# Optimization experiments

Measured on AMD Instinct MI355X. Metric: run time of the kernel, lower is better.

## Reference

```python
import jax, jax.numpy as jnp
import numpy as np

SIZE_DICT = 512
DIM_DICT = 256
TEMPERATURE = 0.5
EPS = 1e-10


def setup_inputs() -> dict:
    key = jax.random.key(0)
    k1, k2, k3 = jax.random.split(key, 3)
    bs, dim_z, W, H = 32, DIM_DICT, 32, 32
    z_from_encoder = jax.random.normal(k1, (bs, dim_z, W, H), dtype=jnp.float32)
    kappa_q = jnp.ones((1,), dtype=jnp.float32)
    codebook = jax.random.normal(k2, (SIZE_DICT, DIM_DICT), dtype=jnp.float32)
    gumbel_u = jax.random.uniform(k3, (bs * W * H, SIZE_DICT), dtype=jnp.float32)
    return {"z_from_encoder": z_from_encoder, "kappa_q": kappa_q,
            "codebook": codebook, "gumbel_u": gumbel_u, "flg_train": 1}


def reference(z_from_encoder, kappa_q, codebook, gumbel_u, flg_train):
    bs, dim_z, W, H = z_from_encoder.shape
    # [bs, dim_z, W, H] -> [bs*W*H, dim_z]
    z_flat = jnp.transpose(z_from_encoder, (0, 2, 3, 1)).reshape(-1, dim_z)
    kq = jnp.clip(kappa_q, 1e-5, 1e5)  # scalar-ish [1]
    # L2-normalize codebook rows
    cb = codebook / jnp.linalg.norm(codebook, axis=1, keepdims=True)
    # logit = -distance = kappa * <z, c>   [N, K]
    logit = kq * (z_flat @ cb.T)
    logit = logit - jnp.max(logit, axis=-1, keepdims=True)
    logit = jnp.clip(logit, -50.0, 50.0)
    probabilities = jax.nn.softmax(logit, axis=-1)
    log_probabilities = jax.nn.log_softmax(logit, axis=-1)
    # training path: gumbel-softmax relaxation
    g = -jnp.log(-jnp.log(gumbel_u + EPS) + EPS)
    encodings = jax.nn.softmax((logit + g) / TEMPERATURE, axis=-1)
    z_quantized = (encodings @ cb).reshape(bs, W, H, dim_z)
    avg_probs = jnp.mean(jax.lax.stop_gradient(probabilities), axis=0)
    z_to_decoder = jnp.transpose(z_quantized, (0, 3, 1, 2))
    kld_discrete = jnp.sum(probabilities * log_probabilities) / bs
    kld_continuous = jnp.mean(
        jnp.sum(z_from_encoder * (z_from_encoder - z_to_decoder) * kq[0],
                axis=(1, 2, 3)))
    loss = kld_discrete + kld_continuous
    avg_probs = jnp.clip(avg_probs, 1e-10, None)
    perplexity = jnp.exp(-jnp.sum(avg_probs * jnp.log(avg_probs + 1e-10)))
    return z_to_decoder, loss, perplexity
```

## Files before the change

### kernel.cpp

```cpp
#include <hip/hip_runtime.h>
#include <stdint.h>


typedef float v4f __attribute__((ext_vector_type(4)));
typedef short v8s __attribute__((ext_vector_type(8)));
typedef short v4s __attribute__((ext_vector_type(4)));

#define ZA_STR 264
#define L2_STR 520
#define EC_STR 40

__device__ __forceinline__ uint16_t f2bf(float x) {
  uint32_t u = __float_as_uint(x);
  u = u + 0x7fffu + ((u >> 16) & 1u);
  return (uint16_t)(u >> 16);
}
__device__ __forceinline__ float bf2f(uint16_t h) {
  return __uint_as_float(((uint32_t)h) << 16);
}


__global__ __launch_bounds__(64) void vq_prep0(const float* __restrict__ cb,
                                               char* __restrict__ ws) {
  const int blk = blockIdx.x, t = threadIdx.x;
  float* shadow = (float*)(ws + 524288);
  float* scal   = (float*)(ws + 557056);
  float* rnorm  = (float*)(ws + 557072);
  if (blk < 512) {
    float s = 0.f;
#pragma unroll
    for (int i = 0; i < 4; i++) { const float v = cb[blk * 256 + t + 64 * i]; s += v * v; }
#pragma unroll
    for (int mm = 1; mm < 64; mm <<= 1) s += __shfl_xor(s, mm, 64);
    if (t == 0) rnorm[blk] = 1.0f / sqrtf(s);
  } else if (blk < 528) {
    const int j = blk - 512;
#pragma unroll
    for (int i = 0; i < 8; i++) shadow[j * 512 + t + 64 * i] = 0.f;
  } else {
    if (t < 3) scal[t] = 0.f;
  }
}

__global__ __launch_bounds__(256) void vq_prep1(const float* __restrict__ cb,
                                                char* __restrict__ ws) {
  const int b = blockIdx.x, t = threadIdx.x;
  uint16_t* cbn2 = (uint16_t*)ws;
  uint16_t* cbt2 = (uint16_t*)(ws + 262144);
  const float* rnorm = (const float*)(ws + 557072);
  union { v8s v; uint16_t u[8]; } pk;
  if (b < 64) {
    const int g = b * 256 + t;
    const int code = g >> 5, dch = g & 31;
    const float rn = rnorm[code];
    const float4 f0 = *(const float4*)(cb + code * 256 + dch * 8);
    const float4 f1 = *(const float4*)(cb + code * 256 + dch * 8 + 4);
    pk.u[0] = f2bf(f0.x * rn); pk.u[1] = f2bf(f0.y * rn);
    pk.u[2] = f2bf(f0.z * rn); pk.u[3] = f2bf(f0.w * rn);
    pk.u[4] = f2bf(f1.x * rn); pk.u[5] = f2bf(f1.y * rn);
    pk.u[6] = f2bf(f1.z * rn); pk.u[7] = f2bf(f1.w * rn);
    const int w = code >> 7, ct = (code >> 4) & 7, mcol = code & 15;
    const int ks = dch >> 2, q3 = dch & 3;
    *(v8s*)(cbn2 + ((ks * 8 + ct) * 4 + w) * 512 + (q3 * 16 + mcol) * 8) = pk.v;
  } else {
    const int g = (b - 64) * 256 + t;
    const int cgroup = g >> 8, d = g & 255;
#pragma unroll
    for (int j = 0; j < 8; j++) {
      const int c = cgroup * 8 + j;
      pk.u[j] = f2bf(cb[c * 256 + d] * rnorm[c]);
    }
    const int cc = cgroup >> 2, qq = cgroup & 3;
    const int wd = d >> 6, nt = (d >> 4) & 3, md = d & 15;
    *(v8s*)(cbt2 + ((cc * 4 + nt) * 4 + wd) * 512 + (qq * 16 + md) * 8) = pk.v;
  }
}

__global__ __launch_bounds__(256, 4) void vq_main(const float* __restrict__ z,
                                                  const float* __restrict__ kappa,
                                                  const float* __restrict__ gum,
                                                  char* __restrict__ ws,
                                                  float* __restrict__ out) {
  __shared__ char s_A[33280];
  __shared__ char s_B[5120];
  __shared__ float s_M[32], s_rS[32], s_kd[32], s_rSe[32], s_red[8];

  const int t = threadIdx.x;
  const int w = t >> 6, lane = t & 63, q = lane >> 4, m = lane & 15;
  const int bi = blockIdx.x, b = bi >> 5, wh0 = (bi & 31) << 5;
  const int R0 = bi << 5;

  const uint16_t* cbn2 = (const uint16_t*)ws;
  const uint16_t* cbt2 = (const uint16_t*)(ws + 262144);
  float* shadow = (float*)(ws + 524288);
  float* scal   = (float*)(ws + 557056);

  uint16_t* za  = (uint16_t*)s_A;
  uint16_t* l2s = (uint16_t*)s_A;
  float* s_pm = (float*)s_B;
  float* s_pS = (float*)s_B + 128;
  float* s_pT = (float*)s_B + 256;
  short* s_ec = (short*)s_B;

  const float kq = fminf(fmaxf(kappa[0], 1e-5f), 1e5f);

  const int row = t >> 3, c4 = (t & 7) << 2;
  const float* gbase = gum + (size_t)(R0 + row) * 512 + c4;

  {
    float zs = 0.f;
    const int whb = (t & 7) << 2, dT = t >> 3;
    const float* zb = z + ((size_t)b << 18) + wh0 + whb;
#pragma unroll
    for (int s = 0; s < 8; s++) {
      const int d = dT + (s << 5);
      const float4 v = *(const float4*)(zb + (d << 10));
      zs += v.x * v.x + v.y * v.y + v.z * v.z + v.w * v.w;
      za[(whb + 0) * ZA_STR + d] = f2bf(v.x);
      za[(whb + 1) * ZA_STR + d] = f2bf(v.y);
      za[(whb + 2) * ZA_STR + d] = f2bf(v.z);
      za[(whb + 3) * ZA_STR + d] = f2bf(v.w);
    }
#pragma unroll
    for (int mm = 1; mm < 64; mm <<= 1) zs += __shfl_xor(zs, mm, 64);
    if (lane == 0) s_red[w] = zs;
  }

  float4 gq[4];
#pragma unroll
  for (int i = 0; i < 4; i++) gq[i] = *(const float4*)(gbase + (i << 5));

  __syncthreads();
  if (t == 0) atomicAdd(&scal[1], s_red[0] + s_red[1] + s_red[2] + s_red[3]);

  v4f acc0[8], acc1[8];
#pragma unroll
  for (int i = 0; i < 8; i++) { acc0[i] = (v4f)0.f; acc1[i] = (v4f)0.f; }
  {
    const uint16_t* bp  = cbn2 + (w << 9) + (lane << 3);
    const uint16_t* a0p = za + m * ZA_STR;
    const uint16_t* a1p = za + (m + 16) * ZA_STR;
#pragma unroll
    for (int ks = 0; ks < 8; ks++) {
      const v8s a0 = *(const v8s*)(a0p + (ks << 5) + (q << 3));
      const v8s a1 = *(const v8s*)(a1p + (ks << 5) + (q << 3));
#pragma unroll
      for (int ct = 0; ct < 8; ct++) {
        const v8s bf = *(const v8s*)(bp + (((ks << 3) + ct) << 11));
        acc0[ct] = __builtin_amdgcn_mfma_f32_16x16x32_bf16(a0, bf, acc0[ct], 0, 0, 0);
        acc1[ct] = __builtin_amdgcn_mfma_f32_16x16x32_bf16(a1, bf, acc1[ct], 0, 0, 0);
      }
    }
  }
#pragma unroll
  for (int i = 0; i < 8; i++) { acc0[i] *= kq; acc1[i] *= kq; }

  {
    auto stats_half = [&](v4f (&acc)[8], int half) {
#pragma unroll
      for (int reg = 0; reg < 4; reg++) {
        float mx = -1e30f;
#pragma unroll
        for (int ct = 0; ct < 8; ct++) mx = fmaxf(mx, acc[ct][reg]);
#pragma unroll
        for (int mm = 1; mm < 16; mm <<= 1) mx = fmaxf(mx, __shfl_xor(mx, mm, 64));
        float S = 0.f, T = 0.f;
#pragma unroll
        for (int ct = 0; ct < 8; ct++) {
          const float d = acc[ct][reg] - mx;
          const float e = __expf(d);
          S += e; T += d * e;
        }
#pragma unroll
        for (int mm = 1; mm < 16; mm <<= 1) { S += __shfl_xor(S, mm, 64); T += __shfl_xor(T, mm, 64); }
        if (m == 0) {
          const int r = half * 16 + q * 4 + reg;
          s_pm[(w << 5) + r] = mx; s_pS[(w << 5) + r] = S; s_pT[(w << 5) + r] = T;
        }
      }
    };
    stats_half(acc0, 0);
    stats_half(acc1, 1);
  }
  __syncthreads();
  if (t < 32) {
    float M = s_pm[t];
    M = fmaxf(M, s_pm[32 + t]); M = fmaxf(M, s_pm[64 + t]); M = fmaxf(M, s_pm[96 + t]);
    float S = 0.f, T = 0.f;
#pragma unroll
    for (int ww = 0; ww < 4; ww++) {
      const float dm = s_pm[ww * 32 + t] - M;
      const float al = __expf(dm);
      S += s_pS[ww * 32 + t] * al;
      T += (s_pT[ww * 32 + t] + dm * s_pS[ww * 32 + t]) * al;
    }
    const float rS = 1.0f / S;
    s_M[t] = M; s_rS[t] = rS; s_kd[t] = T * rS - __logf(S);
  }
  __syncthreads();

  {
    const int c0 = w << 7;
    float colacc[8];
#pragma unroll
    for (int i = 0; i < 8; i++) colacc[i] = 0.f;
    auto pass2_half = [&](v4f (&acc)[8], int half) {
#pragma unroll
      for (int reg = 0; reg < 4; reg++) {
        const int r = half * 16 + q * 4 + reg;
        const float Mr = s_M[r], rSr = s_rS[r];
        uint16_t* lrow = l2s + r * L2_STR + c0 + m;
#pragma unroll
        for (int ct = 0; ct < 8; ct++) {
          const float d = fmaxf(acc[ct][reg] - Mr, -50.0f);
          const float e = __expf(d);
          colacc[ct] += e * rSr;
          lrow[ct << 4] = f2bf(d);
        }
      }
    };
    pass2_half(acc0, 0);
    pass2_half(acc1, 1);
#pragma unroll
    for (int i = 0; i < 8; i++) {
      colacc[i] += __shfl_xor(colacc[i], 16, 64);
      colacc[i] += __shfl_xor(colacc[i], 32, 64);
    }
    if (q == 0) {
      float* sh = shadow + ((bi & 15) << 9) + c0 + m;
#pragma unroll
      for (int i = 0; i < 8; i++) atomicAdd(&sh[i << 4], colacc[i]);
    }
    if (w == 0) {
      float kd = s_kd[lane & 31];
#pragma unroll
      for (int mm = 1; mm < 64; mm <<= 1) kd += __shfl_xor(kd, mm, 64);
      if (lane == 0) atomicAdd(&scal[0], 0.5f * kd);
    }
  }
  __syncthreads();

  const float mxr = s_M[row];
  float se = 0.f, ce = 0.f;
  v4f acc2a[4], acc2b[4];
#pragma unroll
  for (int i = 0; i < 4; i++) { acc2a[i] = (v4f)0.f; acc2b[i] = (v4f)0.f; }

  auto compute_chunk = [&](int cc) {
    const int buf = cc & 1;
    const float4 u = gq[cc & 3];
    const float uu[4] = {u.x, u.y, u.z, u.w};
    union { v4s v; uint16_t h[4]; } lv, eb;
    lv.v = *(const v4s*)(l2s + row * L2_STR + (cc << 5) + c4);
#pragma unroll
    for (int i = 0; i < 4; i++) {
      const float l2 = bf2f(lv.h[i]);
      const float L = -__logf(uu[i] + 1e-10f) + 1e-10f;
      const float er = __expf(2.0f * (l2 - __logf(L)));
      se += er; ce += er * (l2 + mxr);
      eb.h[i] = f2bf(er);
    }
    *(v4s*)(s_ec + buf * 1280 + row * EC_STR + c4) = eb.v;
    if (cc + 4 < 16) gq[cc & 3] = *(const float4*)(gbase + ((cc + 4) << 5));
  };
  auto mfma_chunk = [&](int cc) {
    const int buf = cc & 1;
    const v8s a0 = *(const v8s*)(s_ec + buf * 1280 + m * EC_STR + (q << 3));
    const v8s a1 = *(const v8s*)(s_ec + buf * 1280 + (m + 16) * EC_STR + (q << 3));
    const uint16_t* bp2 = cbt2 + (cc << 13) + (w << 9) + (lane << 3);
#pragma unroll
    for (int nt = 0; nt < 4; nt++) {
      const v8s bf = *(const v8s*)(bp2 + (nt << 11));
      acc2a[nt] = __builtin_amdgcn_mfma_f32_16x16x32_bf16(a0, bf, acc2a[nt], 0, 0, 0);
      acc2b[nt] = __builtin_amdgcn_mfma_f32_16x16x32_bf16(a1, bf, acc2b[nt], 0, 0, 0);
    }
  };

  compute_chunk(0);
  __syncthreads();
#pragma unroll
  for (int cc = 0; cc < 16; cc++) {
    mfma_chunk(cc);
    if (cc < 15) compute_chunk(cc + 1);
    __syncthreads();
  }

#pragma unroll
  for (int mm = 1; mm < 8; mm <<= 1) { se += __shfl_xor(se, mm, 64); ce += __shfl_xor(ce, mm, 64); }
  {
    float cr = ((t & 7) == 0) ? (ce / se) : 0.f;
#pragma unroll
    for (int mm = 8; mm < 64; mm <<= 1) cr += __shfl_xor(cr, mm, 64);
    if (lane == 0) s_red[w] = cr;
    if ((t & 7) == 0) s_rSe[row] = 1.0f / se;
  }
  __syncthreads();
  if (t == 0) atomicAdd(&scal[2], s_red[0] + s_red[1] + s_red[2] + s_red[3]);

  {
    float* ob = out + ((size_t)b << 18) + wh0;
    const int d0 = w << 6;
    float rsA[4], rsB[4];
#pragma unroll
    for (int reg = 0; reg < 4; reg++) {
      rsA[reg] = s_rSe[q * 4 + reg];
      rsB[reg] = s_rSe[16 + q * 4 + reg];
    }
#pragma unroll
    for (int nt = 0; nt < 4; nt++) {
      const int d = d0 + (nt << 4) + m;
#pragma unroll
      for (int reg = 0; reg < 4; reg++) {
        ob[(d << 10) + q * 4 + reg]      = acc2a[nt][reg] * rsA[reg];
        ob[(d << 10) + 16 + q * 4 + reg] = acc2b[nt][reg] * rsB[reg];
      }
    }
  }
}

__global__ __launch_bounds__(512) void vq_final(const float* __restrict__ kappa,
                                                char* __restrict__ ws,
                                                float* __restrict__ out) {
  __shared__ float red[8];
  const int t = threadIdx.x;
  const float* shadow = (const float*)(ws + 524288);
  const float* scal   = (const float*)(ws + 557056);
  float s = 0.f;
#pragma unroll
  for (int j = 0; j < 16; j++) s += shadow[(j << 9) + t];
  float avg = fmaxf(s * (1.0f / 32768.0f), 1e-10f);
  float term = avg * __logf(avg + 1e-10f);
#pragma unroll
  for (int mm = 1; mm < 64; mm <<= 1) term += __shfl_xor(term, mm, 64);
  if ((t & 63) == 0) red[t >> 6] = term;
  __syncthreads();
  if (t == 0) {
    float H = 0.f;
#pragma unroll
    for (int i = 0; i < 8; i++) H += red[i];
    const float perpl = __expf(-H);
    const float kq = fminf(fmaxf(kappa[0], 1e-5f), 1e5f);
    const float loss = (scal[0] + kq * scal[1] - scal[2]) * (1.0f / 32.0f);
    out[8388608] = loss;
    out[8388609] = perpl;
  }
}

extern "C" void kernel_launch(void* const* d_in, const int* in_sizes, int n_in,
                              void* d_out, int out_size, void* d_ws, size_t ws_size,
                              hipStream_t stream) {
  const float* z     = (const float*)d_in[0];
  const float* kappa = (const float*)d_in[1];
  const float* cb    = (const float*)d_in[2];
  const float* gum   = (const float*)d_in[3];
  char* ws = (char*)d_ws;
  float* out = (float*)d_out;
  hipLaunchKernelGGL(vq_prep0, dim3(529),  dim3(64),  0, stream, cb, ws);
  hipLaunchKernelGGL(vq_prep1, dim3(128),  dim3(256), 0, stream, cb, ws);
  hipLaunchKernelGGL(vq_main,  dim3(1024), dim3(256), 0, stream, z, kappa, gum, ws, out);
  hipLaunchKernelGGL(vq_final, dim3(1),    dim3(512), 0, stream, kappa, ws, out);
}
```

Before: 207.4 us.

## Store exp logits in LDS and split gumbel pass from MFMA loop

Pass two now stores exp(d) rather than d as bf16, so the gumbel stage computes (e/L)^2 with a divide instead of an exp. The gumbel weights are written back in place into the shared logit buffer in one pass. A single MFMA loop then reads the A operand straight from that buffer, replacing the double-buffered chunk pipeline that issued 16 barriers. The aim is to cut barrier count, LDS traffic and transcendental work, at the cost of losing overlap between VALU and MFMA. ce also needs log(e) to be recomputed, and storing e in bf16 may lose precision for tiny probabilities.

After: 200.6 us. 3.3% less time.

```diff
diff --git a/kernel.cpp b/kernel.cpp
--- a/kernel.cpp
+++ b/kernel.cpp
@@ -8,7 +8,6 @@
 
 #define ZA_STR 264
 #define L2_STR 520
-#define EC_STR 40
 
 __device__ __forceinline__ uint16_t f2bf(float x) {
   uint32_t u = __float_as_uint(x);
@@ -82,7 +81,7 @@
                                                   char* __restrict__ ws,
                                                   float* __restrict__ out) {
   __shared__ char s_A[33280];
-  __shared__ char s_B[5120];
+  __shared__ float s_pm[128], s_pS[128], s_pT[128];
   __shared__ float s_M[32], s_rS[32], s_kd[32], s_rSe[32], s_red[8];
 
   const int t = threadIdx.x;
@@ -97,10 +96,6 @@
 
   uint16_t* za  = (uint16_t*)s_A;
   uint16_t* l2s = (uint16_t*)s_A;
-  float* s_pm = (float*)s_B;
-  float* s_pS = (float*)s_B + 128;
-  float* s_pT = (float*)s_B + 256;
-  short* s_ec = (short*)s_B;
 
   const float kq = fminf(fmaxf(kappa[0], 1e-5f), 1e5f);
 
@@ -215,7 +210,7 @@
           const float d = fmaxf(acc[ct][reg] - Mr, -50.0f);
           const float e = __expf(d);
           colacc[ct] += e * rSr;
-          lrow[ct << 4] = f2bf(d);
+          lrow[ct << 4] = f2bf(e);
         }
       }
     };
@@ -240,54 +235,30 @@
   }
   __syncthreads();
 
-  const float mxr = s_M[row];
-  float se = 0.f, ce = 0.f;
-  v4f acc2a[4], acc2b[4];
-#pragma unroll
-  for (int i = 0; i < 4; i++) { acc2a[i] = (v4f)0.f; acc2b[i] = (v4f)0.f; }
-
-  auto compute_chunk = [&](int cc) {
-    const int buf = cc & 1;
-    const float4 u = gq[cc & 3];
-    const float uu[4] = {u.x, u.y, u.z, u.w};
-    union { v4s v; uint16_t h[4]; } lv, eb;
-    lv.v = *(const v4s*)(l2s + row * L2_STR + (cc << 5) + c4);
-#pragma unroll
-    for (int i = 0; i < 4; i++) {
-      const float l2 = bf2f(lv.h[i]);
-      const float L = -__logf(uu[i] + 1e-10f) + 1e-10f;
-      const float er = __expf(2.0f * (l2 - __logf(L)));
-      se += er; ce += er * (l2 + mxr);
-      eb.h[i] = f2bf(er);
-    }
-    *(v4s*)(s_ec + buf * 1280 + row * EC_STR + c4) = eb.v;
-    if (cc + 4 < 16) gq[cc & 3] = *(const float4*)(gbase + ((cc + 4) << 5));
-  };
-  auto mfma_chunk = [&](int cc) {
-    const int buf = cc & 1;
-    const v8s a0 = *(const v8s*)(s_ec + buf * 1280 + m * EC_STR + (q << 3));
-    const v8s a1 = *(const v8s*)(s_ec + buf * 1280 + (m + 16) * EC_STR + (q << 3));
-    const uint16_t* bp2 = cbt2 + (cc << 13) + (w << 9) + (lane << 3);
-#pragma unroll
-    for (int nt = 0; nt < 4; nt++) {
-      const v8s bf = *(const v8s*)(bp2 + (nt << 11));
-      acc2a[nt] = __builtin_amdgcn_mfma_f32_16x16x32_bf16(a0, bf, acc2a[nt], 0, 0, 0);
-      acc2b[nt] = __builtin_amdgcn_mfma_f32_16x16x32_bf16(a1, bf, acc2b[nt], 0, 0, 0);
-    }
-  };
-
-  compute_chunk(0);
-  __syncthreads();
-#pragma unroll
-  for (int cc = 0; cc < 16; cc++) {
-    mfma_chunk(cc);
-    if (cc < 15) compute_chunk(cc + 1);
-    __syncthreads();
-  }
-
-#pragma unroll
-  for (int mm = 1; mm < 8; mm <<= 1) { se += __shfl_xor(se, mm, 64); ce += __shfl_xor(ce, mm, 64); }
-  {
+  {
+    const float mxr = s_M[row];
+    float se = 0.f, ce = 0.f;
+    union { v4s v; uint16_t h[4]; } ev, rv;
+#pragma unroll
+    for (int i = 0; i < 16; i++) {
+      const float4 u = gq[i & 3];
+      const float uu[4] = {u.x, u.y, u.z, u.w};
+      ev.v = *(const v4s*)(l2s + row * L2_STR + (i << 5) + c4);
+      if (i < 12) gq[i & 3] = *(const float4*)(gbase + ((i + 4) << 5));
+#pragma unroll
+      for (int j = 0; j < 4; j++) {
+        const float e = bf2f(ev.h[j]);
+        const float L = -__logf(uu[j] + 1e-10f) + 1e-10f;
+        const float f = __fdividef(e, L);
+        const float er = f * f;
+        se += er;
+        ce += er * (__logf(e) + mxr);
+        rv.h[j] = f2bf(er);
+      }
+      *(v4s*)(l2s + row * L2_STR + (i << 5) + c4) = rv.v;
+    }
+#pragma unroll
+    for (int mm = 1; mm < 8; mm <<= 1) { se += __shfl_xor(se, mm, 64); ce += __shfl_xor(ce, mm, 64); }
     float cr = ((t & 7) == 0) ? (ce / se) : 0.f;
 #pragma unroll
     for (int mm = 8; mm < 64; mm <<= 1) cr += __shfl_xor(cr, mm, 64);
@@ -296,6 +267,26 @@
   }
   __syncthreads();
   if (t == 0) atomicAdd(&scal[2], s_red[0] + s_red[1] + s_red[2] + s_red[3]);
+
+  v4f acc2a[4], acc2b[4];
+#pragma unroll
+  for (int i = 0; i < 4; i++) { acc2a[i] = (v4f)0.f; acc2b[i] = (v4f)0.f; }
+  {
+    const uint16_t* a0p = l2s + m * L2_STR;
+    const uint16_t* a1p = l2s + (m + 16) * L2_STR;
+#pragma unroll
+    for (int cc = 0; cc < 16; cc++) {
+      const v8s a0 = *(const v8s*)(a0p + (cc << 5) + (q << 3));
+      const v8s a1 = *(const v8s*)(a1p + (cc << 5) + (q << 3));
+      const uint16_t* bp2 = cbt2 + (cc << 13) + (w << 9) + (lane << 3);
+#pragma unroll
+      for (int nt = 0; nt < 4; nt++) {
+        const v8s bf = *(const v8s*)(bp2 + (nt << 11));
+        acc2a[nt] = __builtin_amdgcn_mfma_f32_16x16x32_bf16(a0, bf, acc2a[nt], 0, 0, 0);
+        acc2b[nt] = __builtin_amdgcn_mfma_f32_16x16x32_bf16(a1, bf, acc2b[nt], 0, 0, 0);
+      }
+    }
+  }
 
   {
     float* ob = out + ((size_t)b << 18) + wh0;
```
